# Kernel optimization log

Measured on AMD Instinct MI355X. Metric: run time of the kernel, lower is better.

Reference implementation:

```python
import jax, jax.numpy as jnp
import numpy as np
from math import sqrt

D_MODEL = 768
D_T = 256
N_HEADS = 12
HEAD_DIM = D_MODEL // N_HEADS
SCALE = sqrt(HEAD_DIM)


def setup_inputs() -> dict:
    key = jax.random.key(0)
    ks = jax.random.split(key, 11)
    b, l = 8, 1024
    inv = 1.0 / sqrt(D_MODEL)
    inv_t = 1.0 / sqrt(D_T)
    return {
        "x": jax.random.normal(ks[0], (b, l, D_MODEL), dtype=jnp.float32),
        "t": jax.random.normal(ks[1], (b, D_T), dtype=jnp.float32),
        "rel_pos_bias": jax.random.normal(ks[2], (N_HEADS, l, l), dtype=jnp.float32),
        # torch Linear weights: [out_features, in_features]
        "Wx_q": jax.random.normal(ks[3], (D_MODEL, D_MODEL), dtype=jnp.float32) * inv,
        "Wx_k": jax.random.normal(ks[4], (D_MODEL, D_MODEL), dtype=jnp.float32) * inv,
        "Wx_v": jax.random.normal(ks[5], (D_MODEL, D_MODEL), dtype=jnp.float32) * inv,
        "Wt_q": jax.random.normal(ks[6], (D_MODEL, D_T), dtype=jnp.float32) * inv_t,
        "Wt_k": jax.random.normal(ks[7], (D_MODEL, D_T), dtype=jnp.float32) * inv_t,
        "Wt_v": jax.random.normal(ks[8], (D_MODEL, D_T), dtype=jnp.float32) * inv_t,
        "W_o": jax.random.normal(ks[9], (D_MODEL, D_MODEL), dtype=jnp.float32) * inv,
        "b_o": jax.random.normal(ks[10], (D_MODEL,), dtype=jnp.float32) * 0.01,
    }


def _split_heads(y):
    # [b, l, n*d] -> [b, n, l, d]
    b, l, _ = y.shape
    return y.reshape(b, l, N_HEADS, HEAD_DIM).transpose(0, 2, 1, 3)


def reference(x, t, rel_pos_bias, Wx_q, Wx_k, Wx_v, Wt_q, Wt_k, Wt_v, W_o, b_o):
    # time-conditioned QKV: per-batch additive shift broadcast over seq
    q = _split_heads(x @ Wx_q.T + (t @ Wt_q.T)[:, None, :])
    k = _split_heads(x @ Wx_k.T + (t @ Wt_k.T)[:, None, :])
    v = _split_heads(x @ Wx_v.T + (t @ Wt_v.T)[:, None, :])
    attn = jnp.einsum("bnld,bnmd->bnlm", q, k) / SCALE
    attn = attn + rel_pos_bias  # [n,l,l] broadcasts over batch
    probs = jax.nn.softmax(attn, axis=-1)
    o = jnp.einsum("bnlm,bnmd->bnld", probs, v)
    b, _, l, _ = o.shape
    o = o.transpose(0, 2, 1, 3).reshape(b, l, D_MODEL)
    return o @ W_o.T + b_o
```

## Files before the change

kernel.cpp:

```cpp
#include <hip/hip_runtime.h>
#include <hip/hip_bf16.h>
#include <stdint.h>

typedef __bf16 bf16_t;
typedef __attribute__((ext_vector_type(8))) __bf16 bf16x8;
typedef __attribute__((ext_vector_type(4))) __bf16 bf16x4;
typedef __attribute__((ext_vector_type(4))) float f32x4;

#define DEVI __device__ __forceinline__

DEVI void gll16(const void* g, void* lds_base_wave_uniform) {
  __builtin_amdgcn_global_load_lds(
      (const __attribute__((address_space(1))) uint32_t*)(uintptr_t)g,
      (__attribute__((address_space(3))) uint32_t*)(uintptr_t)lds_base_wave_uniform,
      16, 0, 0);
}

__global__ void cvt_f32_to_bf16(const float* __restrict__ src, bf16_t* __restrict__ dst, int n) {
  int i = (blockIdx.x * blockDim.x + threadIdx.x) * 4;
  if (i >= n) return;
  float4 v = *(const float4*)(src + i);
  bf16x4 o = {(bf16_t)v.x, (bf16_t)v.y, (bf16_t)v.z, (bf16_t)v.w};
  *(bf16x4*)(dst + i) = o;
}

__global__ void shift_kernel(const float* __restrict__ t,
                             const float* __restrict__ wtq,
                             const float* __restrict__ wtk,
                             const float* __restrict__ wtv,
                             float* __restrict__ shift) {
  int idx = blockIdx.x * blockDim.x + threadIdx.x;
  if (idx >= 8 * 2304) return;
  int b = idx / 2304, n = idx % 2304;
  const float* w = (n < 768) ? (wtq + (size_t)n * 256)
                 : (n < 1536) ? (wtk + (size_t)(n - 768) * 256)
                              : (wtv + (size_t)(n - 1536) * 256);
  const float4* tv = (const float4*)(t + (size_t)b * 256);
  const float4* wv = (const float4*)w;
  float acc = 0.f;
#pragma unroll 8
  for (int i = 0; i < 64; i++) {
    float4 a = tv[i], c = wv[i];
    acc += a.x * c.x + a.y * c.y + a.z * c.z + a.w * c.w;
  }
  shift[idx] = acc;
}

template <int MODE>
__global__ __launch_bounds__(256, 2) void gemm_bt(
    const bf16_t* __restrict__ A, const bf16_t* __restrict__ B,
    const float* __restrict__ add, void* __restrict__ Cout,
    int M, int N, int K) {
  __shared__ alignas(16) bf16_t As[128 * 32];
  __shared__ alignas(16) bf16_t Bs[128 * 32];
  const int t = threadIdx.x, l = t & 63, w = t >> 6;
  const int wr = w >> 1, wc = w & 1;
  const int bm = blockIdx.x, bn = blockIdx.y;

  f32x4 acc[4][4] = {};

  const int srow = t >> 2;
  const int scol = (t & 3) * 8;
  const bf16_t* Ab = A + ((size_t)bm * 128 + srow) * K + scol;
  const bf16_t* Bb = B + ((size_t)bn * 128 + srow) * K + scol;
  char* AsB = (char*)As + w * 1024;
  char* BsB = (char*)Bs + w * 1024;
  const size_t K64 = (size_t)64 * K;

  const int ro = (l & 15) * 32 + (l >> 4) * 8;
  const bf16_t* ApA = As + (wr * 64) * 32 + ro;
  const bf16_t* BpB = Bs + (wc * 64) * 32 + ro;

  for (int k0 = 0; k0 < K; k0 += 32) {
    __syncthreads();
    gll16(Ab + k0, AsB);
    gll16(Ab + K64 + k0, AsB + 4096);
    gll16(Bb + k0, BsB);
    gll16(Bb + K64 + k0, BsB + 4096);
    __syncthreads();
    bf16x8 af[4], bfr[4];
#pragma unroll
    for (int i = 0; i < 4; i++) {
      af[i]  = *(const bf16x8*)(ApA + i * 16 * 32);
      bfr[i] = *(const bf16x8*)(BpB + i * 16 * 32);
    }
#pragma unroll
    for (int mi = 0; mi < 4; mi++)
#pragma unroll
      for (int ni = 0; ni < 4; ni++)
        acc[mi][ni] = __builtin_amdgcn_mfma_f32_16x16x32_bf16(af[mi], bfr[ni], acc[mi][ni], 0, 0, 0);
  }

  const int row0 = bm * 128 + wr * 64 + (l >> 4) * 4;
  const int col0 = bn * 128 + wc * 64 + (l & 15);
  if (MODE == 0) {
    bf16_t* C = (bf16_t*)Cout;
    const float* sh = add + (size_t)((bm * 128) >> 10) * N;
#pragma unroll
    for (int ni = 0; ni < 4; ni++) {
      const int col = col0 + ni * 16;
      const float s0 = sh[col];
#pragma unroll
      for (int mi = 0; mi < 4; mi++)
#pragma unroll
        for (int i = 0; i < 4; i++)
          C[(size_t)(row0 + mi * 16 + i) * N + col] = (bf16_t)(acc[mi][ni][i] + s0);
    }
  } else {
    float* C = (float*)Cout;
#pragma unroll
    for (int ni = 0; ni < 4; ni++) {
      const int col = col0 + ni * 16;
      const float s0 = add[col];
#pragma unroll
      for (int mi = 0; mi < 4; mi++)
#pragma unroll
        for (int i = 0; i < 4; i++)
          C[(size_t)(row0 + mi * 16 + i) * N + col] = acc[mi][ni][i] + s0;
    }
  }
}

__global__ __launch_bounds__(256, 4) void attn_fused(
    const bf16_t* __restrict__ qkv,
    const float* __restrict__ bias,
    bf16_t* __restrict__ o) {
  const int id = blockIdx.x;
  const int slot = id >> 3;
  const int qt = slot & 15;
  const int grp = (id & 7) + 8 * (slot >> 4);
  const int h = grp % 12, b = grp / 12;
  const int t = threadIdx.x, l = t & 63, w = t >> 6;
  const int s = l & 15, g = l >> 4;

  __shared__ alignas(16) bf16_t Vt[64 * 64];
  __shared__ alignas(16) bf16_t Ps[4][16 * 64];

  const size_t rowb = (size_t)b * 1024;
  const int qrow = qt * 64 + w * 16 + s;

  bf16x8 qf[2];
  {
    const bf16_t* qp = qkv + (rowb + qrow) * 2304 + h * 64 + g * 8;
    qf[0] = *(const bf16x8*)qp;
    qf[1] = *(const bf16x8*)(qp + 32);
  }

  const bf16_t* kbase = qkv + rowb * 2304 + 768 + h * 64 + g * 8;
  const float*  bbase = bias + ((size_t)h << 20) + (size_t)qrow * 1024 + g * 4;

  float m_run = -INFINITY, l_run = 0.f;
  f32x4 oacc[4] = {};
  const float LOG2E = 1.44269504088896f;
  const float C1 = 0.125f * 1.44269504088896f;

  for (int kt = 0; kt < 16; kt++) {
    bf16x8 kf[4][2];
    {
      const bf16_t* kb = kbase + (size_t)(kt * 64 + s) * 2304;
#pragma unroll
      for (int nf = 0; nf < 4; nf++) {
        const bf16_t* kr = kb + (size_t)(nf * 16) * 2304;
        kf[nf][0] = *(const bf16x8*)kr;
        kf[nf][1] = *(const bf16x8*)(kr + 32);
      }
    }
    f32x4 bv[4];
    {
      const float* bb = bbase + kt * 64;
#pragma unroll
      for (int nf = 0; nf < 4; nf++)
        bv[nf] = *(const f32x4*)(bb + nf * 16);
    }
    bf16x8 v0, v1;
    {
      const bf16_t* vp = qkv + (rowb + kt * 64 + l) * 2304 + 1536 + h * 64 + w * 16;
      v0 = *(const bf16x8*)vp;
      v1 = *(const bf16x8*)(vp + 8);
    }

    __syncthreads();
#pragma unroll
    for (int j = 0; j < 16; j++) {
      const int d = w * 16 + j;
      const int addr = d * 64 + (((l >> 3) ^ (d & 7)) * 8) + (l & 7);
      Vt[addr] = (j < 8) ? v0[j] : v1[j - 8];
    }

    f32x4 sv[4];
#pragma unroll
    for (int nf = 0; nf < 4; nf++) {
      f32x4 z = {0.f, 0.f, 0.f, 0.f};
      z = __builtin_amdgcn_mfma_f32_16x16x32_bf16(kf[nf][0], qf[0], z, 0, 0, 0);
      z = __builtin_amdgcn_mfma_f32_16x16x32_bf16(kf[nf][1], qf[1], z, 0, 0, 0);
      sv[nf] = z;
    }

    float lg[4][4];
#pragma unroll
    for (int nf = 0; nf < 4; nf++)
#pragma unroll
      for (int i = 0; i < 4; i++)
        lg[nf][i] = fmaf(sv[nf][i], C1, bv[nf][i] * LOG2E);

    float mx = fmaxf(fmaxf(fmaxf(lg[0][0], lg[0][1]), fmaxf(lg[0][2], lg[0][3])),
                     fmaxf(fmaxf(lg[1][0], lg[1][1]), fmaxf(lg[1][2], lg[1][3])));
    mx = fmaxf(mx, fmaxf(fmaxf(fmaxf(lg[2][0], lg[2][1]), fmaxf(lg[2][2], lg[2][3])),
                         fmaxf(fmaxf(lg[3][0], lg[3][1]), fmaxf(lg[3][2], lg[3][3]))));
    mx = fmaxf(mx, __shfl_xor(mx, 16));
    mx = fmaxf(mx, __shfl_xor(mx, 32));

    if (!__all(mx - m_run <= 8.0f)) {
      const float mnew = fmaxf(m_run, mx);
      const float alpha = exp2f(m_run - mnew);
      m_run = mnew;
      l_run *= alpha;
#pragma unroll
      for (int i = 0; i < 4; i++) {
        const float a_pv = __shfl(alpha, g * 4 + i);
#pragma unroll
        for (int nf2 = 0; nf2 < 4; nf2++) oacc[nf2][i] *= a_pv;
      }
    }

    float rs = 0.f;
#pragma unroll
    for (int nf = 0; nf < 4; nf++)
#pragma unroll
      for (int i = 0; i < 4; i++) {
        lg[nf][i] = exp2f(lg[nf][i] - m_run);
        rs += lg[nf][i];
      }
    rs += __shfl_xor(rs, 16);
    rs += __shfl_xor(rs, 32);
    l_run += rs;

    bf16_t* Pw = Ps[w];
    {
      char* pb = (char*)Pw + s * 128 + (g & 1) * 8;
#pragma unroll
      for (int nf = 0; nf < 4; nf++) {
        bf16x4 pk = {(bf16_t)lg[nf][0], (bf16_t)lg[nf][1], (bf16_t)lg[nf][2], (bf16_t)lg[nf][3]};
        *(bf16x4*)(pb + ((2 * nf + (g >> 1)) ^ (s & 7)) * 16) = pk;
      }
    }
    bf16x8 pf[2];
#pragma unroll
    for (int c = 0; c < 2; c++)
      pf[c] = *(const bf16x8*)((char*)Pw + s * 128 + ((4 * c + g) ^ (s & 7)) * 16);

    __syncthreads();

#pragma unroll
    for (int nf2 = 0; nf2 < 4; nf2++) {
      const int d = nf2 * 16 + s;
      const bf16_t* vb = Vt + d * 64;
      bf16x8 vf0 = *(const bf16x8*)(vb + ((g ^ (d & 7)) * 8));
      bf16x8 vf1 = *(const bf16x8*)(vb + (((g + 4) ^ (d & 7)) * 8));
      oacc[nf2] = __builtin_amdgcn_mfma_f32_16x16x32_bf16(pf[0], vf0, oacc[nf2], 0, 0, 0);
      oacc[nf2] = __builtin_amdgcn_mfma_f32_16x16x32_bf16(pf[1], vf1, oacc[nf2], 0, 0, 0);
    }
  }

#pragma unroll
  for (int i = 0; i < 4; i++) {
    const float inv = 1.0f / __shfl(l_run, g * 4 + i);
    const size_t row = rowb + qt * 64 + w * 16 + g * 4 + i;
#pragma unroll
    for (int nf2 = 0; nf2 < 4; nf2++)
      o[row * 768 + h * 64 + nf2 * 16 + s] = (bf16_t)(oacc[nf2][i] * inv);
  }
}

extern "C" void kernel_launch(void* const* d_in, const int* in_sizes, int n_in,
                              void* d_out, int out_size, void* d_ws, size_t ws_size,
                              hipStream_t stream) {
  const float* x    = (const float*)d_in[0];
  const float* tin  = (const float*)d_in[1];
  const float* bias = (const float*)d_in[2];
  const float* Wxq  = (const float*)d_in[3];
  const float* Wxk  = (const float*)d_in[4];
  const float* Wxv  = (const float*)d_in[5];
  const float* Wtq  = (const float*)d_in[6];
  const float* Wtk  = (const float*)d_in[7];
  const float* Wtv  = (const float*)d_in[8];
  const float* Wo   = (const float*)d_in[9];
  const float* bo   = (const float*)d_in[10];
  float* out = (float*)d_out;

  char* ws = (char*)d_ws;
  bf16_t* x_bf    = (bf16_t*)(ws);
  bf16_t* wcat    = (bf16_t*)(ws + 12582912);
  bf16_t* wo_bf   = (bf16_t*)(ws + 16121856);
  float*  shift   = (float*) (ws + 17301504);
  bf16_t* qkvb    = (bf16_t*)(ws + 17375232);
  bf16_t* obuf    = (bf16_t*)(ws + 55123968);

  const int W = 768 * 768;
  cvt_f32_to_bf16<<<6144, 256, 0, stream>>>(x, x_bf, 8192 * 768);
  cvt_f32_to_bf16<<<576, 256, 0, stream>>>(Wxq, wcat, W);
  cvt_f32_to_bf16<<<576, 256, 0, stream>>>(Wxk, wcat + W, W);
  cvt_f32_to_bf16<<<576, 256, 0, stream>>>(Wxv, wcat + 2 * W, W);
  cvt_f32_to_bf16<<<576, 256, 0, stream>>>(Wo, wo_bf, W);
  shift_kernel<<<72, 256, 0, stream>>>(tin, Wtq, Wtk, Wtv, shift);
  gemm_bt<0><<<dim3(64, 18), 256, 0, stream>>>(x_bf, wcat, shift, qkvb, 8192, 2304, 768);
  attn_fused<<<1536, 256, 0, stream>>>(qkvb, bias, obuf);
  gemm_bt<1><<<dim3(64, 6), 256, 0, stream>>>(obuf, wo_bf, bo, out, 8192, 768, 768);
}
```

Measured before the change: 374.8 us.

## Double-buffer K and bias tiles in LDS via async loads, convert bias to bf16

Converts the relative-position bias to bf16, pre-scaled by log2(e), in a new conversion kernel. The attention kernel now stages K and bias tiles into double-buffered LDS using direct global-to-LDS loads and prefetches V two tiles ahead. Explicit waitcnt and barriers pipeline the next tile's loads with the current tile's MFMA and softmax work, and MFMA sections get raised priority. This costs more LDS (occupancy bound drops from 4 to 2 blocks), an extra full pass over the bias tensor each call, and bf16 rounding of the bias.

Result: faster. 316.3 us (-15.6%).

```diff
diff --git a/kernel.cpp b/kernel.cpp
--- a/kernel.cpp
+++ b/kernel.cpp
@@ -21,6 +21,15 @@
   if (i >= n) return;
   float4 v = *(const float4*)(src + i);
   bf16x4 o = {(bf16_t)v.x, (bf16_t)v.y, (bf16_t)v.z, (bf16_t)v.w};
+  *(bf16x4*)(dst + i) = o;
+}
+
+__global__ void cvt_scale_bf16(const float* __restrict__ src, bf16_t* __restrict__ dst, int n) {
+  int i = (blockIdx.x * blockDim.x + threadIdx.x) * 4;
+  if (i >= n) return;
+  const float s = 1.44269504088896f;
+  float4 v = *(const float4*)(src + i);
+  bf16x4 o = {(bf16_t)(v.x * s), (bf16_t)(v.y * s), (bf16_t)(v.z * s), (bf16_t)(v.w * s)};
   *(bf16x4*)(dst + i) = o;
 }
 
@@ -121,9 +130,9 @@
   }
 }
 
-__global__ __launch_bounds__(256, 4) void attn_fused(
+__global__ __launch_bounds__(256, 2) void attn_fused(
     const bf16_t* __restrict__ qkv,
-    const float* __restrict__ bias,
+    const bf16_t* __restrict__ biasb,
     bf16_t* __restrict__ o) {
   const int id = blockIdx.x;
   const int slot = id >> 3;
@@ -131,13 +140,15 @@
   const int grp = (id & 7) + 8 * (slot >> 4);
   const int h = grp % 12, b = grp / 12;
   const int t = threadIdx.x, l = t & 63, w = t >> 6;
-  const int s = l & 15, g = l >> 4;
-
-  __shared__ alignas(16) bf16_t Vt[64 * 64];
+  const int sl = l & 15, g = l >> 4;
+
+  __shared__ alignas(16) bf16_t Ks[2][64 * 64];
+  __shared__ alignas(16) bf16_t Bi[2][64 * 64];
+  __shared__ alignas(16) bf16_t Vt[2][64 * 64];
   __shared__ alignas(16) bf16_t Ps[4][16 * 64];
 
   const size_t rowb = (size_t)b * 1024;
-  const int qrow = qt * 64 + w * 16 + s;
+  const int qrow = qt * 64 + w * 16 + sl;
 
   bf16x8 qf[2];
   {
@@ -145,63 +156,95 @@
     qf[0] = *(const bf16x8*)qp;
     qf[1] = *(const bf16x8*)(qp + 32);
   }
-
-  const bf16_t* kbase = qkv + rowb * 2304 + 768 + h * 64 + g * 8;
-  const float*  bbase = bias + ((size_t)h << 20) + (size_t)qrow * 1024 + g * 4;
-
-  float m_run = -INFINITY, l_run = 0.f;
-  f32x4 oacc[4] = {};
-  const float LOG2E = 1.44269504088896f;
-  const float C1 = 0.125f * 1.44269504088896f;
-
-  for (int kt = 0; kt < 16; kt++) {
-    bf16x8 kf[4][2];
-    {
-      const bf16_t* kb = kbase + (size_t)(kt * 64 + s) * 2304;
-#pragma unroll
-      for (int nf = 0; nf < 4; nf++) {
-        const bf16_t* kr = kb + (size_t)(nf * 16) * 2304;
-        kf[nf][0] = *(const bf16x8*)kr;
-        kf[nf][1] = *(const bf16x8*)(kr + 32);
-      }
-    }
-    f32x4 bv[4];
-    {
-      const float* bb = bbase + kt * 64;
-#pragma unroll
-      for (int nf = 0; nf < 4; nf++)
-        bv[nf] = *(const f32x4*)(bb + nf * 16);
-    }
-    bf16x8 v0, v1;
-    {
-      const bf16_t* vp = qkv + (rowb + kt * 64 + l) * 2304 + 1536 + h * 64 + w * 16;
-      v0 = *(const bf16x8*)vp;
-      v1 = *(const bf16x8*)(vp + 8);
-    }
-
-    __syncthreads();
+  __builtin_amdgcn_sched_barrier(0);
+
+  const int st_row = w * 16 + (l >> 3);
+  const int st_chk = (l & 7) ^ (l >> 3);
+  const bf16_t* ksrc = qkv + rowb * 2304 + 768 + h * 64;
+  const bf16_t* bsrc = biasb + ((size_t)h << 20) + (size_t)(qt * 64) * 1024;
+
+  auto STAGE = [&](int buf, int kt2) {
+    const bf16_t* k0 = ksrc + (size_t)(kt2 * 64 + st_row) * 2304 + st_chk * 8;
+    gll16(k0,            (char*)Ks[buf] + w * 2048);
+    gll16(k0 + 8 * 2304, (char*)Ks[buf] + w * 2048 + 1024);
+    const bf16_t* b0 = bsrc + (size_t)st_row * 1024 + kt2 * 64 + st_chk * 8;
+    gll16(b0,            (char*)Bi[buf] + w * 2048);
+    gll16(b0 + 8 * 1024, (char*)Bi[buf] + w * 2048 + 1024);
+  };
+  auto VLOAD = [&](int kt2, bf16x8& a, bf16x8& bq) {
+    const bf16_t* vp = qkv + (rowb + kt2 * 64 + l) * 2304 + 1536 + h * 64 + w * 16;
+    a = *(const bf16x8*)vp;
+    bq = *(const bf16x8*)(vp + 8);
+  };
+  auto VSCAT = [&](int buf, const bf16x8& a, const bf16x8& bq) {
 #pragma unroll
     for (int j = 0; j < 16; j++) {
       const int d = w * 16 + j;
       const int addr = d * 64 + (((l >> 3) ^ (d & 7)) * 8) + (l & 7);
-      Vt[addr] = (j < 8) ? v0[j] : v1[j - 8];
+      Vt[buf][addr] = (j < 8) ? a[j] : bq[j - 8];
+    }
+  };
+
+  float m_run = -INFINITY, l_run = 0.f;
+  f32x4 oacc[4] = {};
+  const float C1 = 0.125f * 1.44269504088896f;
+
+  bf16x8 va0, va1, vb0, vb1;
+
+  VLOAD(0, va0, va1);
+  __builtin_amdgcn_sched_barrier(0);
+  STAGE(0, 0);
+  __builtin_amdgcn_sched_barrier(0);
+  VLOAD(1, vb0, vb1);
+  __builtin_amdgcn_sched_barrier(0);
+  VSCAT(0, va0, va1);
+  asm volatile("s_waitcnt vmcnt(2) lgkmcnt(0)" ::: "memory");
+  __builtin_amdgcn_s_barrier();
+  __builtin_amdgcn_sched_barrier(0);
+
+#pragma unroll 2
+  for (int kt = 0; kt < 16; kt++) {
+    const int cur = kt & 1, nxt = cur ^ 1;
+
+    if (kt + 1 < 16) {
+      STAGE(nxt, kt + 1);
+      __builtin_amdgcn_sched_barrier(0);
+    }
+    if (kt + 2 < 16) {
+      if (cur == 0) VLOAD(kt + 2, va0, va1);
+      else          VLOAD(kt + 2, vb0, vb1);
+      __builtin_amdgcn_sched_barrier(0);
+    }
+    if (kt + 1 < 16) {
+      if (cur == 0) VSCAT(nxt, vb0, vb1);
+      else          VSCAT(nxt, va0, va1);
     }
 
     f32x4 sv[4];
+    __builtin_amdgcn_s_setprio(1);
 #pragma unroll
     for (int nf = 0; nf < 4; nf++) {
+      const char* base = (const char*)Ks[cur] + (16 * nf + sl) * 128;
+      bf16x8 kf0 = *(const bf16x8*)(base + ((g ^ (sl & 7)) * 16));
+      bf16x8 kf1 = *(const bf16x8*)(base + (((4 + g) ^ (sl & 7)) * 16));
       f32x4 z = {0.f, 0.f, 0.f, 0.f};
-      z = __builtin_amdgcn_mfma_f32_16x16x32_bf16(kf[nf][0], qf[0], z, 0, 0, 0);
-      z = __builtin_amdgcn_mfma_f32_16x16x32_bf16(kf[nf][1], qf[1], z, 0, 0, 0);
+      z = __builtin_amdgcn_mfma_f32_16x16x32_bf16(kf0, qf[0], z, 0, 0, 0);
+      z = __builtin_amdgcn_mfma_f32_16x16x32_bf16(kf1, qf[1], z, 0, 0, 0);
       sv[nf] = z;
     }
+    __builtin_amdgcn_s_setprio(0);
 
     float lg[4][4];
-#pragma unroll
-    for (int nf = 0; nf < 4; nf++)
-#pragma unroll
-      for (int i = 0; i < 4; i++)
-        lg[nf][i] = fmaf(sv[nf][i], C1, bv[nf][i] * LOG2E);
+    {
+      const char* bb = (const char*)Bi[cur] + (w * 16 + sl) * 128 + (g & 1) * 8;
+#pragma unroll
+      for (int nf = 0; nf < 4; nf++) {
+        bf16x4 bq = *(const bf16x4*)(bb + (((2 * nf + (g >> 1)) ^ (sl & 7)) * 16));
+#pragma unroll
+        for (int i = 0; i < 4; i++)
+          lg[nf][i] = fmaf(sv[nf][i], C1, (float)bq[i]);
+      }
+    }
 
     float mx = fmaxf(fmaxf(fmaxf(lg[0][0], lg[0][1]), fmaxf(lg[0][2], lg[0][3])),
                      fmaxf(fmaxf(lg[1][0], lg[1][1]), fmaxf(lg[1][2], lg[1][3])));
@@ -237,29 +280,36 @@
 
     bf16_t* Pw = Ps[w];
     {
-      char* pb = (char*)Pw + s * 128 + (g & 1) * 8;
+      char* pb = (char*)Pw + sl * 128 + (g & 1) * 8;
 #pragma unroll
       for (int nf = 0; nf < 4; nf++) {
         bf16x4 pk = {(bf16_t)lg[nf][0], (bf16_t)lg[nf][1], (bf16_t)lg[nf][2], (bf16_t)lg[nf][3]};
-        *(bf16x4*)(pb + ((2 * nf + (g >> 1)) ^ (s & 7)) * 16) = pk;
+        *(bf16x4*)(pb + ((2 * nf + (g >> 1)) ^ (sl & 7)) * 16) = pk;
       }
     }
     bf16x8 pf[2];
 #pragma unroll
     for (int c = 0; c < 2; c++)
-      pf[c] = *(const bf16x8*)((char*)Pw + s * 128 + ((4 * c + g) ^ (s & 7)) * 16);
-
-    __syncthreads();
-
+      pf[c] = *(const bf16x8*)((char*)Pw + sl * 128 + ((4 * c + g) ^ (sl & 7)) * 16);
+
+    __builtin_amdgcn_s_setprio(1);
 #pragma unroll
     for (int nf2 = 0; nf2 < 4; nf2++) {
-      const int d = nf2 * 16 + s;
-      const bf16_t* vb = Vt + d * 64;
+      const int d = nf2 * 16 + sl;
+      const bf16_t* vb = Vt[cur] + d * 64;
       bf16x8 vf0 = *(const bf16x8*)(vb + ((g ^ (d & 7)) * 8));
       bf16x8 vf1 = *(const bf16x8*)(vb + (((g + 4) ^ (d & 7)) * 8));
       oacc[nf2] = __builtin_amdgcn_mfma_f32_16x16x32_bf16(pf[0], vf0, oacc[nf2], 0, 0, 0);
       oacc[nf2] = __builtin_amdgcn_mfma_f32_16x16x32_bf16(pf[1], vf1, oacc[nf2], 0, 0, 0);
     }
+    __builtin_amdgcn_s_setprio(0);
+
+    if (kt + 1 < 16) {
+      if (kt + 2 < 16) asm volatile("s_waitcnt vmcnt(2) lgkmcnt(0)" ::: "memory");
+      else             asm volatile("s_waitcnt vmcnt(0) lgkmcnt(0)" ::: "memory");
+      __builtin_amdgcn_s_barrier();
+      __builtin_amdgcn_sched_barrier(0);
+    }
   }
 
 #pragma unroll
@@ -268,7 +318,7 @@
     const size_t row = rowb + qt * 64 + w * 16 + g * 4 + i;
 #pragma unroll
     for (int nf2 = 0; nf2 < 4; nf2++)
-      o[row * 768 + h * 64 + nf2 * 16 + s] = (bf16_t)(oacc[nf2][i] * inv);
+      o[row * 768 + h * 64 + nf2 * 16 + sl] = (bf16_t)(oacc[nf2][i] * inv);
   }
 }
 
@@ -295,6 +345,7 @@
   float*  shift   = (float*) (ws + 17301504);
   bf16_t* qkvb    = (bf16_t*)(ws + 17375232);
   bf16_t* obuf    = (bf16_t*)(ws + 55123968);
+  bf16_t* bias_bf = (bf16_t*)(ws + 67706880);
 
   const int W = 768 * 768;
   cvt_f32_to_bf16<<<6144, 256, 0, stream>>>(x, x_bf, 8192 * 768);
@@ -302,8 +353,9 @@
   cvt_f32_to_bf16<<<576, 256, 0, stream>>>(Wxk, wcat + W, W);
   cvt_f32_to_bf16<<<576, 256, 0, stream>>>(Wxv, wcat + 2 * W, W);
   cvt_f32_to_bf16<<<576, 256, 0, stream>>>(Wo, wo_bf, W);
+  cvt_scale_bf16<<<12288, 256, 0, stream>>>(bias, bias_bf, 12 * 1024 * 1024);
   shift_kernel<<<72, 256, 0, stream>>>(tin, Wtq, Wtk, Wtv, shift);
   gemm_bt<0><<<dim3(64, 18), 256, 0, stream>>>(x_bf, wcat, shift, qkvb, 8192, 2304, 768);
-  attn_fused<<<1536, 256, 0, stream>>>(qkvb, bias, obuf);
+  attn_fused<<<1536, 256, 0, stream>>>(qkvb, bias_bf, obuf);
   gemm_bt<1><<<dim3(64, 6), 256, 0, stream>>>(obuf, wo_bf, bo, out, 8192, 768, 768);
 }
```
